# Performance work log

Measured on AMD Instinct MI355X. Metric: run time of the kernel, lower is better.

Reference implementation:

```python
import jax, jax.numpy as jnp
import numpy as np
import math

HEAD_DIM = 64           # d_model // n_heads // 2
N_HEADS = 8
LAMBDA_INIT = 0.8 - 0.6 * math.exp(-0.3 * 6)  # depth=6
EPS = 1e-5


def setup_inputs() -> dict:
    key = jax.random.key(0)
    ks = jax.random.split(key, 8)
    B, T, S = 2, 2048, 2048
    return {
        "queries": jax.random.normal(ks[0], (B, 2 * N_HEADS, T, HEAD_DIM), jnp.float32),
        "keys": jax.random.normal(ks[1], (B, 2 * N_HEADS, S, HEAD_DIM), jnp.float32),
        "values": jax.random.normal(ks[2], (B, N_HEADS, S, 2 * HEAD_DIM), jnp.float32),
        "lambda_q1": 0.02 * jax.random.normal(ks[3], (HEAD_DIM,), jnp.float32),
        "lambda_k1": 0.02 * jax.random.normal(ks[4], (HEAD_DIM,), jnp.float32),
        "lambda_q2": 0.02 * jax.random.normal(ks[5], (HEAD_DIM,), jnp.float32),
        "lambda_k2": 0.02 * jax.random.normal(ks[6], (HEAD_DIM,), jnp.float32),
        "subln_weight": jnp.ones((2 * HEAD_DIM,), jnp.float32),
        "tgt_len": 2048,
        "src_len": 2048,
        "attn_mask": jnp.zeros((1,), jnp.bool_),
    }


def reference(queries, keys, values, lambda_q1, lambda_k1, lambda_q2, lambda_k2,
              subln_weight, tgt_len, src_len, attn_mask):
    B = queries.shape[0]
    scaling = HEAD_DIM ** -0.5
    q = queries * scaling
    # [B, 2H, T, S]
    attn_w = jnp.einsum('bhtd,bhsd->bhts', q, keys)
    attn_w = jax.nn.softmax(attn_w.astype(jnp.float32), axis=-1).astype(queries.dtype)
    lam1 = jnp.exp(jnp.sum(lambda_q1 * lambda_k1))
    lam2 = jnp.exp(jnp.sum(lambda_q2 * lambda_k2))
    lam_full = lam1 - lam2 + LAMBDA_INIT
    attn_w = attn_w.reshape(B, N_HEADS, 2, tgt_len, src_len)
    attn_w = attn_w[:, :, 0] - lam_full * attn_w[:, :, 1]   # [B, H, T, S]
    attn = jnp.einsum('bhts,bhse->bhte', attn_w, values)    # [B, H, T, 2*HEAD_DIM]
    # RMSNorm over last dim
    normed = attn * jax.lax.rsqrt(jnp.mean(jnp.square(attn.astype(jnp.float32)), axis=-1, keepdims=True) + EPS).astype(attn.dtype)
    normed = normed * subln_weight
    out = normed * (1.0 - LAMBDA_INIT)
    out = out.transpose(0, 2, 1, 3).reshape(B, tgt_len, N_HEADS * 2 * HEAD_DIM)
    return out
```

## Files before the change

kernel.cpp:

```cpp
#include <hip/hip_runtime.h>
#include <math.h>


#define NT    2048
#define D     64
#define DV    128
#define TQ    64
#define TS    32
#define NROUND (NT / (2 * TS))

#define LAMBDA_INIT 0.70082066706704814f
#define OUT_SCALE   0.29917933293295186f
#define QSCALE      0.18033688011112042f

typedef __attribute__((ext_vector_type(8)))  short    short8;
typedef __attribute__((ext_vector_type(4)))  short    short4v;
typedef __attribute__((ext_vector_type(8)))  _Float16 half8;
typedef __attribute__((ext_vector_type(2)))  __fp16   fp16x2;
typedef __attribute__((ext_vector_type(4)))  float    f32x4;
typedef unsigned short u16;
typedef unsigned int   u32;

#define MFMAH(a, b, c)  __builtin_amdgcn_mfma_f32_16x16x32_f16(a, b, c, 0, 0, 0)
#define MFMA16(a, b, c) __builtin_amdgcn_mfma_f32_16x16x32_bf16(a, b, c, 0, 0, 0)

#if __has_builtin(__builtin_amdgcn_exp2f)
#define EXP2F(x) __builtin_amdgcn_exp2f(x)
#else
#define EXP2F(x) exp2f(x)
#endif

union Hu { half8 v; _Float16 e[8]; u16 s[8]; short8 sv; };

__device__ __forceinline__ u16 f2h(float x) {
    Hu u; u.e[0] = (_Float16)x; return u.s[0];
}

__device__ __forceinline__ void glds16(const u16* g, const u16* l) {
    __builtin_amdgcn_global_load_lds(
        (const __attribute__((address_space(1))) void*)g,
        (__attribute__((address_space(3))) void*)l, 16, 0, 0);
}

__global__ __launch_bounds__(256) void prep_kv(
    const float* __restrict__ Kg, const float* __restrict__ Vg,
    const float* __restrict__ lq1, const float* __restrict__ lk1,
    const float* __restrict__ lq2, const float* __restrict__ lk2,
    u16* __restrict__ Kf, u16* __restrict__ Vf, float* __restrict__ lamw)
{
    __shared__ u16 th[64 * 136];
    const int bid = blockIdx.x;
    const int t   = threadIdx.x;
    if (bid < 2048) {
        const int idx = (bid * 256 + t) * 8;
        const float4 a = *(const float4*)(Kg + idx);
        const float4 b = *(const float4*)(Kg + idx + 4);
        Hu H;
        H.e[0] = (_Float16)a.x; H.e[1] = (_Float16)a.y;
        H.e[2] = (_Float16)a.z; H.e[3] = (_Float16)a.w;
        H.e[4] = (_Float16)b.x; H.e[5] = (_Float16)b.y;
        H.e[6] = (_Float16)b.z; H.e[7] = (_Float16)b.w;
        *(short8*)(Kf + idx) = H.sv;
        return;
    }
    if (bid == 2048) {
        if (t == 0) {
            float t1 = 0.f, t2 = 0.f;
            for (int i = 0; i < D; ++i) {
                t1 = fmaf(lq1[i], lk1[i], t1);
                t2 = fmaf(lq2[i], lk2[i], t2);
            }
            lamw[0] = __expf(t1) - __expf(t2) + LAMBDA_INIT;
        }
        return;
    }
    const int i  = bid - 2049;
    const int bh = i >> 5;
    const int eb = (i >> 4) & 1;
    const int sb = i & 15;
    const size_t vbase = (size_t)bh * NT * DV + (size_t)sb * 128 * DV + eb * 64;
    {
        const int r0 = t >> 4;
        const int c4 = (t & 15) * 4;
        #pragma unroll
        for (int rr = 0; rr < 8; ++rr) {
            const int row = r0 + rr * 16;
            const float4 x = *(const float4*)(Vg + vbase + (size_t)row * DV + c4);
            th[(c4 + 0) * 136 + row] = f2h(x.x);
            th[(c4 + 1) * 136 + row] = f2h(x.y);
            th[(c4 + 2) * 136 + row] = f2h(x.z);
            th[(c4 + 3) * 136 + row] = f2h(x.w);
        }
    }
    __syncthreads();
    const int e  = t >> 2;
    const int g  = t & 3;
    const size_t orow = ((size_t)bh * DV + eb * 64 + e) * NT + sb * 128;
    #pragma unroll
    for (int c = 0; c < 4; ++c) {
        Hu o;
        #pragma unroll
        for (int j = 0; j < 8; ++j)
            o.s[j] = th[e * 136 + g * 32 + 4 * c + (j & 3) + 16 * (j >> 2)];
        *(short8*)(Vf + orow + g * 32 + c * 8) = o.sv;
    }
}

struct SmemF {
    union {
        short8 c[4096];
        struct {
            float epi[2][32][132];
            float lbuf[2][2][2][32];
        } e;
    };
};

__global__ __launch_bounds__(512, 4) void diffattn_mfma12(
    const float* __restrict__ Qg,
    const u16* __restrict__ Kf, const u16* __restrict__ Vf,
    const float* __restrict__ lamw,
    const float* __restrict__ Wg, float* __restrict__ Outg)
{
    __shared__ SmemF sm;

    const int tid    = threadIdx.x;
    const int wv     = tid >> 6;
    const int lane   = tid & 63;
    const int quad   = lane >> 4;
    const int lc     = lane & 15;
    const int stripe = wv & 1;
    const int hh     = (wv >> 1) & 1;
    const int ks     = wv >> 2;
    const int wig    = wv & 3;
    const int qt     = blockIdx.x;
    const int bh     = blockIdx.y;
    const int b      = bh >> 3, h = bh & 7;

    const int head2b = b * 16 + 2 * h;
    const int bh8    = b * 8 + h;
    const float lam  = lamw[0];

    half8 qf[2][2];
    {
        const size_t qhead = (size_t)(head2b + hh) * NT * D;
        #pragma unroll
        for (int nq = 0; nq < 2; ++nq) {
            const int row = qt * TQ + stripe * 32 + nq * 16 + lc;
            #pragma unroll
            for (int k0 = 0; k0 < 2; ++k0) {
                const int d0 = k0 * 32 + quad * 8;
                const float4 x = *(const float4*)(Qg + qhead + (size_t)row * D + d0);
                const float4 y = *(const float4*)(Qg + qhead + (size_t)row * D + d0 + 4);
                Hu q;
                q.e[0] = (_Float16)(x.x * QSCALE); q.e[1] = (_Float16)(x.y * QSCALE);
                q.e[2] = (_Float16)(x.z * QSCALE); q.e[3] = (_Float16)(x.w * QSCALE);
                q.e[4] = (_Float16)(y.x * QSCALE); q.e[5] = (_Float16)(y.y * QSCALE);
                q.e[6] = (_Float16)(y.z * QSCALE); q.e[7] = (_Float16)(y.w * QSCALE);
                qf[nq][k0] = q.v;
            }
        }
    }

    f32x4 O_[2][8];
    #pragma unroll
    for (int nq = 0; nq < 2; ++nq)
        #pragma unroll
        for (int nt = 0; nt < 8; ++nt) O_[nq][nt] = (f32x4){0.f, 0.f, 0.f, 0.f};
    float lac[2] = {0.f, 0.f};

    u32 kSrc[2], vSrc[2];
    u32 kLds[2], vLds[2];
    #pragma unroll
    for (int t = 0; t < 2; ++t) {
        const int p   = (wig * 2 + t) * 64 + lane;
        const int hhs = p >> 8;
        const int n   = (p >> 3) & 31;
        const int db  = (p & 7) ^ (n & 7);
        kSrc[t] = (u32)(((head2b + hhs) * NT + n) * D + db * 8);
        kLds[t] = (u32)((ks * 512 + (wig * 2 + t) * 64) * 16);
        const int e = p >> 2;
        const int u = (p & 3) ^ ((e >> 1) & 3);
        vSrc[t] = (u32)((bh8 * DV + e) * NT + u * 8);
        vLds[t] = (u32)((1024 + ks * 512 + (wig * 2 + t) * 64) * 16);
    }
    const u16* ldsu = (const u16*)&sm.c[0];

    #pragma unroll
    for (int t = 0; t < 2; ++t) {
        glds16(Kf + kSrc[t] + (u32)ks * (TS * D), ldsu + (kLds[t] >> 1));
        glds16(Vf + vSrc[t] + (u32)ks * TS,       ldsu + (vLds[t] >> 1));
    }
    __syncthreads();

    u32 kOff[2][2];
    #pragma unroll
    for (int k0 = 0; k0 < 2; ++k0)
        #pragma unroll
        for (int mt = 0; mt < 2; ++mt)
            kOff[k0][mt] = (u32)((ks * 512 + hh * 256 + (mt * 16 + lc) * 8 +
                                  ((4 * k0 + quad) ^ (lc & 7))) * 8);
    u32 vOff[8];
    {
        const int swzv = quad ^ ((lc >> 1) & 3);
        #pragma unroll
        for (int nt = 0; nt < 8; ++nt)
            vOff[nt] = (u32)((1024 + ks * 512 + (nt * 16 + lc) * 4 + swzv) * 8);
    }

    const fp16x2 ones = {(__fp16)1.f, (__fp16)1.f};

    for (int r = 0; r < NROUND; ++r) {
        const u32 bo = ((u32)(r & 1)) << 14;

        if (r < NROUND - 1) {
            const u32 tn = (u32)(2 * (r + 1) + ks);
            const u32 ab = ((u32)((r + 1) & 1)) << 14;
            #pragma unroll
            for (int t = 0; t < 2; ++t) {
                glds16(Kf + kSrc[t] + tn * (TS * D), ldsu + ab + (kLds[t] >> 1));
                glds16(Vf + vSrc[t] + tn * TS,       ldsu + ab + (vLds[t] >> 1));
            }
        }

        f32x4 sf[2][2];
        #pragma unroll
        for (int mt = 0; mt < 2; ++mt)
            #pragma unroll
            for (int nq = 0; nq < 2; ++nq) sf[mt][nq] = (f32x4){0.f, 0.f, 0.f, 0.f};
        #pragma unroll
        for (int k0 = 0; k0 < 2; ++k0) {
            #pragma unroll
            for (int mt = 0; mt < 2; ++mt) {
                const half8 kfr = *(const half8*)(ldsu + bo + kOff[k0][mt]);
                #pragma unroll
                for (int nq = 0; nq < 2; ++nq)
                    sf[mt][nq] = MFMAH(kfr, qf[nq][k0], sf[mt][nq]);
            }
        }

        half8 a8[2];
        #pragma unroll
        for (int nq = 0; nq < 2; ++nq) {
            union { half8 v; fp16x2 h[4]; } a;
            float ls = lac[nq];
            #pragma unroll
            for (int mt = 0; mt < 2; ++mt)
                #pragma unroll
                for (int ip = 0; ip < 2; ++ip) {
                    const float p0 = EXP2F(sf[mt][nq][2 * ip]);
                    const float p1 = EXP2F(sf[mt][nq][2 * ip + 1]);
                    const fp16x2 h2 = __builtin_amdgcn_cvt_pkrtz(p0, p1);
                    a.h[mt * 2 + ip] = h2;
                    ls = __builtin_amdgcn_fdot2(h2, ones, ls, false);
                }
            lac[nq] = ls;
            a8[nq] = a.v;
        }

        #pragma unroll
        for (int nt = 0; nt < 8; ++nt) {
            const half8 vfr = *(const half8*)(ldsu + bo + vOff[nt]);
            #pragma unroll
            for (int nq = 0; nq < 2; ++nq)
                O_[nq][nt] = MFMAH(a8[nq], vfr, O_[nq][nt]);
        }

        __syncthreads();
    }

    {
        float s0 = lac[0], s1 = lac[1];
        s0 += __shfl_xor(s0, 16); s0 += __shfl_xor(s0, 32);
        s1 += __shfl_xor(s1, 16); s1 += __shfl_xor(s1, 32);
        if (quad == 0) {
            sm.e.lbuf[hh][ks][stripe][lc]      = s0;
            sm.e.lbuf[hh][ks][stripe][16 + lc] = s1;
        }
    }
    __syncthreads();
    float coef[2][4];
    #pragma unroll
    for (int nq = 0; nq < 2; ++nq)
        #pragma unroll
        for (int i = 0; i < 4; ++i) {
            const int row = nq * 16 + quad * 4 + i;
            const float lt = sm.e.lbuf[hh][0][stripe][row] +
                             sm.e.lbuf[hh][1][stripe][row];
            coef[nq][i] = (hh == 0) ? (1.f / lt) : (-lam / lt);
        }
    __syncthreads();
    const int pid = hh * 2 + ks;
    #pragma unroll
    for (int p = 0; p < 4; ++p) {
        if (pid == p) {
            #pragma unroll
            for (int nq = 0; nq < 2; ++nq)
                #pragma unroll
                for (int i = 0; i < 4; ++i) {
                    const int row = nq * 16 + quad * 4 + i;
                    #pragma unroll
                    for (int nt = 0; nt < 8; ++nt) {
                        const int col = nt * 16 + lc;
                        const float v = O_[nq][nt][i] * coef[nq][i];
                        if (p == 0) sm.e.epi[stripe][row][col] = v;
                        else        sm.e.epi[stripe][row][col] += v;
                    }
                }
        }
        __syncthreads();
    }
    {
        const int r0 = wv * 8 + (lane >> 3);
        const int st = r0 >> 5, ri = r0 & 31;
        const int e0 = (lane & 7) * 16;
        float x[16];
        float ssq = 0.f;
        #pragma unroll
        for (int m = 0; m < 16; m += 4) {
            const float4 t4 = *(const float4*)&sm.e.epi[st][ri][e0 + m];
            x[m] = t4.x; x[m + 1] = t4.y; x[m + 2] = t4.z; x[m + 3] = t4.w;
            ssq += t4.x * t4.x + t4.y * t4.y + t4.z * t4.z + t4.w * t4.w;
        }
        ssq += __shfl_xor(ssq, 1);
        ssq += __shfl_xor(ssq, 2);
        ssq += __shfl_xor(ssq, 4);
        const float rsq = rsqrtf(ssq * (1.f / 128.f) + 1e-5f) * OUT_SCALE;
        const int rowg = qt * TQ + r0;
        const size_t base =
            ((size_t)b * NT + rowg) * (size_t)(8 * DV) + (size_t)h * DV;
        #pragma unroll
        for (int m = 0; m < 16; m += 4) {
            const float4 w4 = *(const float4*)(Wg + e0 + m);
            float4 o4;
            o4.x = x[m] * rsq * w4.x;
            o4.y = x[m + 1] * rsq * w4.y;
            o4.z = x[m + 2] * rsq * w4.z;
            o4.w = x[m + 3] * rsq * w4.w;
            *(float4*)(Outg + base + e0 + m) = o4;
        }
    }
}

__device__ __forceinline__ unsigned short f2bf(float x) {
    unsigned u = __float_as_uint(x);
    return (unsigned short)((u + 0x7fffu + ((u >> 16) & 1u)) >> 16);
}
__device__ __forceinline__ float bf2f(unsigned short h) {
    return __uint_as_float(((unsigned)h) << 16);
}

struct SmemB {
    union {
        struct {
            short8 kh[2][264];
            short8 kl[2][264];
            short8 vh[516];
            short8 vl[516];
            unsigned short ph[2][2560];
            unsigned short pl[2][2560];
        } L;
        float epi[2][32][132];
    };
};

__global__ __launch_bounds__(256, 2) void diffattn_fb(
    const float* __restrict__ Qg, const float* __restrict__ Kg,
    const float* __restrict__ Vg,
    const float* __restrict__ lq1, const float* __restrict__ lk1,
    const float* __restrict__ lq2, const float* __restrict__ lk2,
    const float* __restrict__ Wg, float* __restrict__ Outg)
{
    __shared__ SmemB sm;
    const int tid = threadIdx.x;
    const int wv = tid >> 6, lane = tid & 63;
    const int quad = lane >> 4, lc = lane & 15;
    const int stripe = wv & 1, hh = wv >> 1;
    const int qt = blockIdx.x, bh = blockIdx.y;
    const int b = bh >> 3, h = bh & 7;
    const size_t koff0 = ((size_t)(b * 16 + 2 * h)) * NT * D;
    const size_t voff  = ((size_t)(b * 8 + h)) * NT * DV;
    float t1 = 0.f, t2 = 0.f;
    for (int i = 0; i < D; ++i) {
        t1 = fmaf(lq1[i], lk1[i], t1);
        t2 = fmaf(lq2[i], lk2[i], t2);
    }
    const float lam = __expf(t1) - __expf(t2) + LAMBDA_INIT;
    short8 qfh[2][2], qfl[2][2];
    {
        const size_t qhead = ((size_t)(b * 16 + 2 * h + hh)) * NT * D;
        #pragma unroll
        for (int mt = 0; mt < 2; ++mt)
            #pragma unroll
            for (int k0 = 0; k0 < 2; ++k0) {
                const int row = qt * TQ + stripe * 32 + mt * 16 + lc;
                const int d0  = k0 * 32 + quad * 8;
                const float4 x = *(const float4*)(Qg + qhead + (size_t)row * D + d0);
                const float4 y = *(const float4*)(Qg + qhead + (size_t)row * D + d0 + 4);
                float f[8] = {x.x, x.y, x.z, x.w, y.x, y.y, y.z, y.w};
                #pragma unroll
                for (int j = 0; j < 8; ++j) {
                    const float v = f[j] * 0.125f;
                    const unsigned short hi = f2bf(v);
                    qfh[mt][k0][j] = (short)hi;
                    qfl[mt][k0][j] = (short)f2bf(v - bf2f(hi));
                }
            }
    }
    f32x4 O_[2][8];
    #pragma unroll
    for (int mt = 0; mt < 2; ++mt)
        #pragma unroll
        for (int nt = 0; nt < 8; ++nt) O_[mt][nt] = (f32x4){0.f, 0.f, 0.f, 0.f};
    float m_[2][4], l_[2][4], a_[2][4];
    #pragma unroll
    for (int mt = 0; mt < 2; ++mt)
        #pragma unroll
        for (int i = 0; i < 4; ++i) { m_[mt][i] = -1e30f; l_[mt][i] = 0.f; }
    const int s_hh = tid >> 7;
    const int s_n  = (tid >> 2) & 31;
    const int s_d0 = (tid & 3) * 16;
    const int s_e0 = tid & 31;
    const int s_s0 = ((tid >> 5) & 7) * 4;
    const int s_sb = s_s0 >> 3;
    const int s_hs = (s_s0 & 4) ? 1 : 0;
    for (int kt = 0; kt < NT / TS; ++kt) {
        const int kb = kt * TS;
        __syncthreads();
        {
            const float* kp = Kg + koff0 + (size_t)s_hh * NT * D +
                              (size_t)(kb + s_n) * D + s_d0;
            const float4 x0 = ((const float4*)kp)[0];
            const float4 x1 = ((const float4*)kp)[1];
            const float4 x2 = ((const float4*)kp)[2];
            const float4 x3 = ((const float4*)kp)[3];
            float f[16] = {x0.x, x0.y, x0.z, x0.w, x1.x, x1.y, x1.z, x1.w,
                           x2.x, x2.y, x2.z, x2.w, x3.x, x3.y, x3.z, x3.w};
            short8 c0h, c0l, c1h, c1l;
            #pragma unroll
            for (int j = 0; j < 8; ++j) {
                unsigned short hi = f2bf(f[j]);
                c0h[j] = (short)hi; c0l[j] = (short)f2bf(f[j] - bf2f(hi));
                hi = f2bf(f[8 + j]);
                c1h[j] = (short)hi; c1l[j] = (short)f2bf(f[8 + j] - bf2f(hi));
            }
            const int db0 = s_d0 >> 3;
            sm.L.kh[s_hh][db0 * 33 + s_n]       = c0h;
            sm.L.kl[s_hh][db0 * 33 + s_n]       = c0l;
            sm.L.kh[s_hh][(db0 + 1) * 33 + s_n] = c1h;
            sm.L.kl[s_hh][(db0 + 1) * 33 + s_n] = c1l;
        }
        {
            #pragma unroll
            for (int j = 0; j < 4; ++j) {
                const int e = s_e0 + 32 * j;
                float f[4];
                #pragma unroll
                for (int i = 0; i < 4; ++i)
                    f[i] = Vg[voff + (size_t)(kb + s_s0 + i) * DV + e];
                short4v hi4, lo4;
                #pragma unroll
                for (int i = 0; i < 4; ++i) {
                    const unsigned short hi = f2bf(f[i]);
                    hi4[i] = (short)hi;
                    lo4[i] = (short)f2bf(f[i] - bf2f(hi));
                }
                ((short4v*)&sm.L.vh[s_sb * 129 + e])[s_hs] = hi4;
                ((short4v*)&sm.L.vl[s_sb * 129 + e])[s_hs] = lo4;
            }
        }
        __syncthreads();
        f32x4 s_f[2][2];
        #pragma unroll
        for (int mt = 0; mt < 2; ++mt)
            #pragma unroll
            for (int nt = 0; nt < 2; ++nt) s_f[mt][nt] = (f32x4){0.f, 0.f, 0.f, 0.f};
        #pragma unroll
        for (int k0 = 0; k0 < 2; ++k0)
            #pragma unroll
            for (int nt = 0; nt < 2; ++nt) {
                const short8 kh = sm.L.kh[hh][(4 * k0 + quad) * 33 + nt * 16 + lc];
                const short8 kl = sm.L.kl[hh][(4 * k0 + quad) * 33 + nt * 16 + lc];
                #pragma unroll
                for (int mt = 0; mt < 2; ++mt) {
                    s_f[mt][nt] = MFMA16(qfh[mt][k0], kh, s_f[mt][nt]);
                    s_f[mt][nt] = MFMA16(qfl[mt][k0], kh, s_f[mt][nt]);
                    s_f[mt][nt] = MFMA16(qfh[mt][k0], kl, s_f[mt][nt]);
                }
            }
        #pragma unroll
        for (int mt = 0; mt < 2; ++mt)
            #pragma unroll
            for (int i = 0; i < 4; ++i) {
                const float v0 = s_f[mt][0][i], v1 = s_f[mt][1][i];
                float mx = fmaxf(v0, v1);
                mx = fmaxf(mx, __shfl_xor(mx, 1));
                mx = fmaxf(mx, __shfl_xor(mx, 2));
                mx = fmaxf(mx, __shfl_xor(mx, 4));
                mx = fmaxf(mx, __shfl_xor(mx, 8));
                const float mn = fmaxf(m_[mt][i], mx);
                const float al = __expf(m_[mt][i] - mn);
                const float p0 = __expf(v0 - mn);
                const float p1 = __expf(v1 - mn);
                float rs = p0 + p1;
                rs += __shfl_xor(rs, 1);
                rs += __shfl_xor(rs, 2);
                rs += __shfl_xor(rs, 4);
                rs += __shfl_xor(rs, 8);
                l_[mt][i] = l_[mt][i] * al + rs;
                m_[mt][i] = mn;
                a_[mt][i] = al;
                const int r = stripe * 32 + mt * 16 + quad * 4 + i;
                const unsigned short h0 = f2bf(p0);
                sm.L.ph[hh][r * 40 + lc]      = h0;
                sm.L.pl[hh][r * 40 + lc]      = f2bf(p0 - bf2f(h0));
                const unsigned short h1 = f2bf(p1);
                sm.L.ph[hh][r * 40 + 16 + lc] = h1;
                sm.L.pl[hh][r * 40 + 16 + lc] = f2bf(p1 - bf2f(h1));
            }
        __syncthreads();
        #pragma unroll
        for (int mt = 0; mt < 2; ++mt)
            #pragma unroll
            for (int nt = 0; nt < 8; ++nt)
                #pragma unroll
                for (int i = 0; i < 4; ++i) O_[mt][nt][i] *= a_[mt][i];
        short8 pah[2], pal[2];
        #pragma unroll
        for (int mt = 0; mt < 2; ++mt) {
            const int r = stripe * 32 + mt * 16 + lc;
            pah[mt] = *(const short8*)&sm.L.ph[hh][r * 40 + quad * 8];
            pal[mt] = *(const short8*)&sm.L.pl[hh][r * 40 + quad * 8];
        }
        #pragma unroll
        for (int nt = 0; nt < 8; ++nt) {
            const short8 vh = sm.L.vh[quad * 129 + nt * 16 + lc];
            const short8 vl = sm.L.vl[quad * 129 + nt * 16 + lc];
            #pragma unroll
            for (int mt = 0; mt < 2; ++mt) {
                O_[mt][nt] = MFMA16(pah[mt], vh, O_[mt][nt]);
                O_[mt][nt] = MFMA16(pal[mt], vh, O_[mt][nt]);
                O_[mt][nt] = MFMA16(pah[mt], vl, O_[mt][nt]);
            }
        }
    }
    __syncthreads();
    if (hh == 1) {
        #pragma unroll
        for (int mt = 0; mt < 2; ++mt)
            #pragma unroll
            for (int i = 0; i < 4; ++i) {
                const float inv = lam / l_[mt][i];
                const int r = mt * 16 + quad * 4 + i;
                #pragma unroll
                for (int nt = 0; nt < 8; ++nt)
                    sm.epi[stripe][r][nt * 16 + lc] = O_[mt][nt][i] * inv;
            }
    }
    __syncthreads();
    if (hh == 0) {
        float wvv[8];
        #pragma unroll
        for (int nt = 0; nt < 8; ++nt) wvv[nt] = Wg[nt * 16 + lc];
        #pragma unroll
        for (int mt = 0; mt < 2; ++mt)
            #pragma unroll
            for (int i = 0; i < 4; ++i) {
                const float inv1 = 1.f / l_[mt][i];
                const int r = mt * 16 + quad * 4 + i;
                float od[8];
                float ss = 0.f;
                #pragma unroll
                for (int nt = 0; nt < 8; ++nt) {
                    od[nt] = O_[mt][nt][i] * inv1 - sm.epi[stripe][r][nt * 16 + lc];
                    ss = fmaf(od[nt], od[nt], ss);
                }
                ss += __shfl_xor(ss, 1);
                ss += __shfl_xor(ss, 2);
                ss += __shfl_xor(ss, 4);
                ss += __shfl_xor(ss, 8);
                const float rsq = rsqrtf(ss * (1.f / 128.f) + 1e-5f) * OUT_SCALE;
                const int rowg = qt * TQ + stripe * 32 + r;
                const size_t base =
                    ((size_t)b * NT + rowg) * (size_t)(8 * DV) + (size_t)h * DV;
                #pragma unroll
                for (int nt = 0; nt < 8; ++nt)
                    Outg[base + nt * 16 + lc] = od[nt] * rsq * wvv[nt];
            }
    }
}

extern "C" void kernel_launch(void* const* d_in, const int* in_sizes, int n_in,
                              void* d_out, int out_size, void* d_ws, size_t ws_size,
                              hipStream_t stream) {
    const float* Q   = (const float*)d_in[0];
    const float* K   = (const float*)d_in[1];
    const float* V   = (const float*)d_in[2];
    const float* lq1 = (const float*)d_in[3];
    const float* lk1 = (const float*)d_in[4];
    const float* lq2 = (const float*)d_in[5];
    const float* lk2 = (const float*)d_in[6];
    const float* W   = (const float*)d_in[7];
    float* Out = (float*)d_out;
    const size_t NEED = 2ull * 4194304ull * sizeof(u16) + 16;
    if (ws_size >= NEED) {
        u16*   Kf   = (u16*)d_ws;
        u16*   Vf   = Kf + 4194304;
        float* lamw = (float*)(Vf + 4194304);
        prep_kv<<<2561, 256, 0, stream>>>(K, V, lq1, lk1, lq2, lk2, Kf, Vf, lamw);
        diffattn_mfma12<<<dim3(NT / TQ, 16), 512, 0, stream>>>(
            Q, Kf, Vf, lamw, W, Out);
    } else {
        diffattn_fb<<<dim3(NT / TQ, 16), 256, 0, stream>>>(
            Q, K, V, lq1, lk1, lq2, lk2, W, Out);
    }
}
```

Before: 169.6 us.

## Pre-swizzle K/V into MFMA fragment order and load directly from global

```diff
diff --git a/kernel.cpp b/kernel.cpp
--- a/kernel.cpp
+++ b/kernel.cpp
@@ -34,12 +34,6 @@
 
 __device__ __forceinline__ u16 f2h(float x) {
     Hu u; u.e[0] = (_Float16)x; return u.s[0];
-}
-
-__device__ __forceinline__ void glds16(const u16* g, const u16* l) {
-    __builtin_amdgcn_global_load_lds(
-        (const __attribute__((address_space(1))) void*)g,
-        (__attribute__((address_space(3))) void*)l, 16, 0, 0);
 }
 
 __global__ __launch_bounds__(256) void prep_kv(
@@ -51,19 +45,50 @@
     __shared__ u16 th[64 * 136];
     const int bid = blockIdx.x;
     const int t   = threadIdx.x;
-    if (bid < 2048) {
-        const int idx = (bid * 256 + t) * 8;
-        const float4 a = *(const float4*)(Kg + idx);
-        const float4 b = *(const float4*)(Kg + idx + 4);
-        Hu H;
-        H.e[0] = (_Float16)a.x; H.e[1] = (_Float16)a.y;
-        H.e[2] = (_Float16)a.z; H.e[3] = (_Float16)a.w;
-        H.e[4] = (_Float16)b.x; H.e[5] = (_Float16)b.y;
-        H.e[6] = (_Float16)b.z; H.e[7] = (_Float16)b.w;
-        *(short8*)(Kf + idx) = H.sv;
+    if (bid < 1024) {
+        const int bh2 = bid >> 5;
+        const int tp  = bid & 31;
+        {
+            const int key = t >> 2;
+            const int d0  = (t & 3) * 16;
+            const float* src =
+                Kg + ((size_t)bh2 * NT + (size_t)tp * 64 + key) * D + d0;
+            const float4 x0 = ((const float4*)src)[0];
+            const float4 x1 = ((const float4*)src)[1];
+            const float4 x2 = ((const float4*)src)[2];
+            const float4 x3 = ((const float4*)src)[3];
+            Hu a, b;
+            a.e[0] = (_Float16)x0.x; a.e[1] = (_Float16)x0.y;
+            a.e[2] = (_Float16)x0.z; a.e[3] = (_Float16)x0.w;
+            a.e[4] = (_Float16)x1.x; a.e[5] = (_Float16)x1.y;
+            a.e[6] = (_Float16)x1.z; a.e[7] = (_Float16)x1.w;
+            b.e[0] = (_Float16)x2.x; b.e[1] = (_Float16)x2.y;
+            b.e[2] = (_Float16)x2.z; b.e[3] = (_Float16)x2.w;
+            b.e[4] = (_Float16)x3.x; b.e[5] = (_Float16)x3.y;
+            b.e[6] = (_Float16)x3.z; b.e[7] = (_Float16)x3.w;
+            *(short8*)(th + key * 80 + d0)     = a.sv;
+            *(short8*)(th + key * 80 + d0 + 8) = b.sv;
+        }
+        __syncthreads();
+        #pragma unroll
+        for (int q = 0; q < 2; ++q) {
+            const int c    = t * 2 + q;
+            const int tt   = c >> 8;
+            const int k0   = (c >> 7) & 1;
+            const int mt   = (c >> 6) & 1;
+            const int lane = c & 63;
+            const int qd   = lane >> 4, lcl = lane & 15;
+            const short8 o =
+                *(const short8*)(th + (tt * 32 + mt * 16 + lcl) * 80 +
+                                 k0 * 32 + qd * 8);
+            const size_t oc =
+                (((size_t)(bh2 * 64 + tp * 2 + tt)) * 4 + k0 * 2 + mt) * 512 +
+                lane * 8;
+            *(short8*)(Kf + oc) = o;
+        }
         return;
     }
-    if (bid == 2048) {
+    if (bid == 1024) {
         if (t == 0) {
             float t1 = 0.f, t2 = 0.f;
             for (int i = 0; i < D; ++i) {
@@ -74,7 +99,7 @@
         }
         return;
     }
-    const int i  = bid - 2049;
+    const int i  = bid - 1025;
     const int bh = i >> 5;
     const int eb = (i >> 4) & 1;
     const int sb = i & 15;
@@ -93,36 +118,37 @@
         }
     }
     __syncthreads();
-    const int e  = t >> 2;
-    const int g  = t & 3;
-    const size_t orow = ((size_t)bh * DV + eb * 64 + e) * NT + sb * 128;
     #pragma unroll
-    for (int c = 0; c < 4; ++c) {
-        Hu o;
+    for (int q = 0; q < 4; ++q) {
+        const int o    = t * 4 + q;
+        const int gt   = o >> 8;
+        const int ntl  = (o >> 6) & 3;
+        const int lane = o & 63;
+        const int cq   = lane >> 4, lcl = lane & 15;
+        const int el   = ntl * 16 + lcl;
+        Hu ov;
         #pragma unroll
         for (int j = 0; j < 8; ++j)
-            o.s[j] = th[e * 136 + g * 32 + 4 * c + (j & 3) + 16 * (j >> 2)];
-        *(short8*)(Vf + orow + g * 32 + c * 8) = o.sv;
+            ov.s[j] = th[el * 136 + gt * 32 + 4 * cq + (j & 3) + 16 * (j >> 2)];
+        const size_t oc =
+            (((size_t)(bh * 64 + sb * 4 + gt)) * 8 + eb * 4 + ntl) * 512 +
+            lane * 8;
+        *(short8*)(Vf + oc) = ov.sv;
     }
 }
 
-struct SmemF {
-    union {
-        short8 c[4096];
-        struct {
-            float epi[2][32][132];
-            float lbuf[2][2][2][32];
-        } e;
-    };
+struct SmemE {
+    float epi[2][32][132];
+    float lbuf[2][2][2][32];
 };
 
-__global__ __launch_bounds__(512, 4) void diffattn_mfma12(
+__global__ __launch_bounds__(512, 4) void diffattn_mfma13(
     const float* __restrict__ Qg,
     const u16* __restrict__ Kf, const u16* __restrict__ Vf,
     const float* __restrict__ lamw,
     const float* __restrict__ Wg, float* __restrict__ Outg)
 {
-    __shared__ SmemF sm;
+    __shared__ SmemE sm;
 
     const int tid    = threadIdx.x;
     const int wv     = tid >> 6;
@@ -132,18 +158,18 @@
     const int stripe = wv & 1;
     const int hh     = (wv >> 1) & 1;
     const int ks     = wv >> 2;
-    const int wig    = wv & 3;
     const int qt     = blockIdx.x;
     const int bh     = blockIdx.y;
     const int b      = bh >> 3, h = bh & 7;
 
     const int head2b = b * 16 + 2 * h;
     const int bh8    = b * 8 + h;
+    const int bh2    = head2b + hh;
     const float lam  = lamw[0];
 
     half8 qf[2][2];
     {
-        const size_t qhead = (size_t)(head2b + hh) * NT * D;
+        const size_t qhead = (size_t)bh2 * NT * D;
         #pragma unroll
         for (int nq = 0; nq < 2; ++nq) {
             const int row = qt * TQ + stripe * 32 + nq * 16 + lc;
@@ -169,75 +195,35 @@
         for (int nt = 0; nt < 8; ++nt) O_[nq][nt] = (f32x4){0.f, 0.f, 0.f, 0.f};
     float lac[2] = {0.f, 0.f};
 
-    u32 kSrc[2], vSrc[2];
-    u32 kLds[2], vLds[2];
-    #pragma unroll
-    for (int t = 0; t < 2; ++t) {
-        const int p   = (wig * 2 + t) * 64 + lane;
-        const int hhs = p >> 8;
-        const int n   = (p >> 3) & 31;
-        const int db  = (p & 7) ^ (n & 7);
-        kSrc[t] = (u32)(((head2b + hhs) * NT + n) * D + db * 8);
-        kLds[t] = (u32)((ks * 512 + (wig * 2 + t) * 64) * 16);
-        const int e = p >> 2;
-        const int u = (p & 3) ^ ((e >> 1) & 3);
-        vSrc[t] = (u32)((bh8 * DV + e) * NT + u * 8);
-        vLds[t] = (u32)((1024 + ks * 512 + (wig * 2 + t) * 64) * 16);
-    }
-    const u16* ldsu = (const u16*)&sm.c[0];
-
-    #pragma unroll
-    for (int t = 0; t < 2; ++t) {
-        glds16(Kf + kSrc[t] + (u32)ks * (TS * D), ldsu + (kLds[t] >> 1));
-        glds16(Vf + vSrc[t] + (u32)ks * TS,       ldsu + (vLds[t] >> 1));
-    }
-    __syncthreads();
-
-    u32 kOff[2][2];
-    #pragma unroll
-    for (int k0 = 0; k0 < 2; ++k0)
-        #pragma unroll
-        for (int mt = 0; mt < 2; ++mt)
-            kOff[k0][mt] = (u32)((ks * 512 + hh * 256 + (mt * 16 + lc) * 8 +
-                                  ((4 * k0 + quad) ^ (lc & 7))) * 8);
-    u32 vOff[8];
-    {
-        const int swzv = quad ^ ((lc >> 1) & 3);
-        #pragma unroll
-        for (int nt = 0; nt < 8; ++nt)
-            vOff[nt] = (u32)((1024 + ks * 512 + (nt * 16 + lc) * 4 + swzv) * 8);
-    }
+    const u32 kbase = (u32)(bh2 * 64) * 2048 + (u32)(lane * 8);
+    const u32 vbase = (u32)(bh8 * 64) * 4096 + (u32)(lane * 8);
 
     const fp16x2 ones = {(__fp16)1.f, (__fp16)1.f};
+    const f32x4  z4   = {0.f, 0.f, 0.f, 0.f};
 
     for (int r = 0; r < NROUND; ++r) {
-        const u32 bo = ((u32)(r & 1)) << 14;
-
-        if (r < NROUND - 1) {
-            const u32 tn = (u32)(2 * (r + 1) + ks);
-            const u32 ab = ((u32)((r + 1) & 1)) << 14;
-            #pragma unroll
-            for (int t = 0; t < 2; ++t) {
-                glds16(Kf + kSrc[t] + tn * (TS * D), ldsu + ab + (kLds[t] >> 1));
-                glds16(Vf + vSrc[t] + tn * TS,       ldsu + ab + (vLds[t] >> 1));
-            }
-        }
+        const u32 t_ = (u32)(2 * r + ks);
+        const u16* kp = Kf + kbase + t_ * 2048;
+        const u16* vp = Vf + vbase + t_ * 4096;
+
+        half8 kfr[2][2];
+        #pragma unroll
+        for (int k0 = 0; k0 < 2; ++k0)
+            #pragma unroll
+            for (int mt = 0; mt < 2; ++mt)
+                kfr[k0][mt] = *(const half8*)(kp + (k0 * 2 + mt) * 512);
 
         f32x4 sf[2][2];
         #pragma unroll
         for (int mt = 0; mt < 2; ++mt)
             #pragma unroll
-            for (int nq = 0; nq < 2; ++nq) sf[mt][nq] = (f32x4){0.f, 0.f, 0.f, 0.f};
-        #pragma unroll
-        for (int k0 = 0; k0 < 2; ++k0) {
-            #pragma unroll
-            for (int mt = 0; mt < 2; ++mt) {
-                const half8 kfr = *(const half8*)(ldsu + bo + kOff[k0][mt]);
-                #pragma unroll
-                for (int nq = 0; nq < 2; ++nq)
-                    sf[mt][nq] = MFMAH(kfr, qf[nq][k0], sf[mt][nq]);
-            }
-        }
+            for (int nq = 0; nq < 2; ++nq)
+                sf[mt][nq] = MFMAH(kfr[0][mt], qf[nq][0], z4);
+        #pragma unroll
+        for (int mt = 0; mt < 2; ++mt)
+            #pragma unroll
+            for (int nq = 0; nq < 2; ++nq)
+                sf[mt][nq] = MFMAH(kfr[1][mt], qf[nq][1], sf[mt][nq]);
 
         half8 a8[2];
         #pragma unroll
@@ -259,14 +245,17 @@
         }
 
         #pragma unroll
-        for (int nt = 0; nt < 8; ++nt) {
-            const half8 vfr = *(const half8*)(ldsu + bo + vOff[nt]);
-            #pragma unroll
-            for (int nq = 0; nq < 2; ++nq)
-                O_[nq][nt] = MFMAH(a8[nq], vfr, O_[nq][nt]);
-        }
-
-        __syncthreads();
+        for (int g = 0; g < 2; ++g) {
+            half8 vfr[4];
+            #pragma unroll
+            for (int n = 0; n < 4; ++n)
+                vfr[n] = *(const half8*)(vp + (g * 4 + n) * 512);
+            #pragma unroll
+            for (int n = 0; n < 4; ++n)
+                #pragma unroll
+                for (int nq = 0; nq < 2; ++nq)
+                    O_[nq][g * 4 + n] = MFMAH(a8[nq], vfr[n], O_[nq][g * 4 + n]);
+        }
     }
 
     {
@@ -274,8 +263,8 @@
         s0 += __shfl_xor(s0, 16); s0 += __shfl_xor(s0, 32);
         s1 += __shfl_xor(s1, 16); s1 += __shfl_xor(s1, 32);
         if (quad == 0) {
-            sm.e.lbuf[hh][ks][stripe][lc]      = s0;
-            sm.e.lbuf[hh][ks][stripe][16 + lc] = s1;
+            sm.lbuf[hh][ks][stripe][lc]      = s0;
+            sm.lbuf[hh][ks][stripe][16 + lc] = s1;
         }
     }
     __syncthreads();
@@ -285,8 +274,8 @@
         #pragma unroll
         for (int i = 0; i < 4; ++i) {
             const int row = nq * 16 + quad * 4 + i;
-            const float lt = sm.e.lbuf[hh][0][stripe][row] +
-                             sm.e.lbuf[hh][1][stripe][row];
+            const float lt = sm.lbuf[hh][0][stripe][row] +
+                             sm.lbuf[hh][1][stripe][row];
             coef[nq][i] = (hh == 0) ? (1.f / lt) : (-lam / lt);
         }
     __syncthreads();
@@ -303,8 +292,8 @@
                     for (int nt = 0; nt < 8; ++nt) {
                         const int col = nt * 16 + lc;
                         const float v = O_[nq][nt][i] * coef[nq][i];
-                        if (p == 0) sm.e.epi[stripe][row][col] = v;
-                        else        sm.e.epi[stripe][row][col] += v;
+                        if (p == 0) sm.epi[stripe][row][col] = v;
+                        else        sm.epi[stripe][row][col] += v;
                     }
                 }
         }
@@ -318,7 +307,7 @@
         float ssq = 0.f;
         #pragma unroll
         for (int m = 0; m < 16; m += 4) {
-            const float4 t4 = *(const float4*)&sm.e.epi[st][ri][e0 + m];
+            const float4 t4 = *(const float4*)&sm.epi[st][ri][e0 + m];
             x[m] = t4.x; x[m + 1] = t4.y; x[m + 2] = t4.z; x[m + 3] = t4.w;
             ssq += t4.x * t4.x + t4.y * t4.y + t4.z * t4.z + t4.w * t4.w;
         }
@@ -607,8 +596,8 @@
         u16*   Kf   = (u16*)d_ws;
         u16*   Vf   = Kf + 4194304;
         float* lamw = (float*)(Vf + 4194304);
-        prep_kv<<<2561, 256, 0, stream>>>(K, V, lq1, lk1, lq2, lk2, Kf, Vf, lamw);
-        diffattn_mfma12<<<dim3(NT / TQ, 16), 512, 0, stream>>>(
+        prep_kv<<<1537, 256, 0, stream>>>(K, V, lq1, lk1, lq2, lk2, Kf, Vf, lamw);
+        diffattn_mfma13<<<dim3(NT / TQ, 16), 512, 0, stream>>>(
             Q, Kf, Vf, lamw, W, Out);
     } else {
         diffattn_fb<<<dim3(NT / TQ, 16), 256, 0, stream>>>(
```

Result: no change. 168.9 us (-0.4%).

## Pre-swizzle V into MFMA fragment order and load it directly from global

Applied to the files above, without the earlier changes.

```diff
diff --git a/kernel.cpp b/kernel.cpp
--- a/kernel.cpp
+++ b/kernel.cpp
@@ -93,22 +93,28 @@
         }
     }
     __syncthreads();
-    const int e  = t >> 2;
-    const int g  = t & 3;
-    const size_t orow = ((size_t)bh * DV + eb * 64 + e) * NT + sb * 128;
-    #pragma unroll
-    for (int c = 0; c < 4; ++c) {
-        Hu o;
+    #pragma unroll
+    for (int q = 0; q < 4; ++q) {
+        const int o    = t * 4 + q;
+        const int gt   = o >> 8;
+        const int ntl  = (o >> 6) & 3;
+        const int lane = o & 63;
+        const int cq   = lane >> 4, lcl = lane & 15;
+        const int el   = ntl * 16 + lcl;
+        Hu ov;
         #pragma unroll
         for (int j = 0; j < 8; ++j)
-            o.s[j] = th[e * 136 + g * 32 + 4 * c + (j & 3) + 16 * (j >> 2)];
-        *(short8*)(Vf + orow + g * 32 + c * 8) = o.sv;
+            ov.s[j] = th[el * 136 + gt * 32 + 4 * cq + (j & 3) + 16 * (j >> 2)];
+        const size_t oc =
+            (((size_t)(bh * 64 + sb * 4 + gt)) * 8 + eb * 4 + ntl) * 512 +
+            lane * 8;
+        *(short8*)(Vf + oc) = ov.sv;
     }
 }
 
 struct SmemF {
     union {
-        short8 c[4096];
+        short8 c[2048];
         struct {
             float epi[2][32][132];
             float lbuf[2][2][2][32];
@@ -116,7 +122,7 @@
     };
 };
 
-__global__ __launch_bounds__(512, 4) void diffattn_mfma12(
+__global__ __launch_bounds__(512, 4) void diffattn_mfma14(
     const float* __restrict__ Qg,
     const u16* __restrict__ Kf, const u16* __restrict__ Vf,
     const float* __restrict__ lamw,
@@ -139,11 +145,12 @@
 
     const int head2b = b * 16 + 2 * h;
     const int bh8    = b * 8 + h;
+    const int bh2    = head2b + hh;
     const float lam  = lamw[0];
 
     half8 qf[2][2];
     {
-        const size_t qhead = (size_t)(head2b + hh) * NT * D;
+        const size_t qhead = (size_t)bh2 * NT * D;
         #pragma unroll
         for (int nq = 0; nq < 2; ++nq) {
             const int row = qt * TQ + stripe * 32 + nq * 16 + lc;
@@ -169,8 +176,8 @@
         for (int nt = 0; nt < 8; ++nt) O_[nq][nt] = (f32x4){0.f, 0.f, 0.f, 0.f};
     float lac[2] = {0.f, 0.f};
 
-    u32 kSrc[2], vSrc[2];
-    u32 kLds[2], vLds[2];
+    u32 kSrc[2];
+    u32 kLds[2];
     #pragma unroll
     for (int t = 0; t < 2; ++t) {
         const int p   = (wig * 2 + t) * 64 + lane;
@@ -179,18 +186,12 @@
         const int db  = (p & 7) ^ (n & 7);
         kSrc[t] = (u32)(((head2b + hhs) * NT + n) * D + db * 8);
         kLds[t] = (u32)((ks * 512 + (wig * 2 + t) * 64) * 16);
-        const int e = p >> 2;
-        const int u = (p & 3) ^ ((e >> 1) & 3);
-        vSrc[t] = (u32)((bh8 * DV + e) * NT + u * 8);
-        vLds[t] = (u32)((1024 + ks * 512 + (wig * 2 + t) * 64) * 16);
     }
     const u16* ldsu = (const u16*)&sm.c[0];
 
     #pragma unroll
-    for (int t = 0; t < 2; ++t) {
+    for (int t = 0; t < 2; ++t)
         glds16(Kf + kSrc[t] + (u32)ks * (TS * D), ldsu + (kLds[t] >> 1));
-        glds16(Vf + vSrc[t] + (u32)ks * TS,       ldsu + (vLds[t] >> 1));
-    }
     __syncthreads();
 
     u32 kOff[2][2];
@@ -200,27 +201,22 @@
         for (int mt = 0; mt < 2; ++mt)
             kOff[k0][mt] = (u32)((ks * 512 + hh * 256 + (mt * 16 + lc) * 8 +
                                   ((4 * k0 + quad) ^ (lc & 7))) * 8);
-    u32 vOff[8];
-    {
-        const int swzv = quad ^ ((lc >> 1) & 3);
-        #pragma unroll
-        for (int nt = 0; nt < 8; ++nt)
-            vOff[nt] = (u32)((1024 + ks * 512 + (nt * 16 + lc) * 4 + swzv) * 8);
-    }
+
+    const u32 vbase = (u32)(bh8 * 64) * 4096 + (u32)(lane * 8);
 
     const fp16x2 ones = {(__fp16)1.f, (__fp16)1.f};
 
     for (int r = 0; r < NROUND; ++r) {
-        const u32 bo = ((u32)(r & 1)) << 14;
+        const u32 bo = ((u32)(r & 1)) << 13;
+        const u32 t_ = (u32)(2 * r + ks);
+        const u16* vp = Vf + vbase + t_ * 4096;
 
         if (r < NROUND - 1) {
             const u32 tn = (u32)(2 * (r + 1) + ks);
-            const u32 ab = ((u32)((r + 1) & 1)) << 14;
-            #pragma unroll
-            for (int t = 0; t < 2; ++t) {
+            const u32 ab = ((u32)((r + 1) & 1)) << 13;
+            #pragma unroll
+            for (int t = 0; t < 2; ++t)
                 glds16(Kf + kSrc[t] + tn * (TS * D), ldsu + ab + (kLds[t] >> 1));
-                glds16(Vf + vSrc[t] + tn * TS,       ldsu + ab + (vLds[t] >> 1));
-            }
         }
 
         f32x4 sf[2][2];
@@ -259,11 +255,18 @@
         }
 
         #pragma unroll
-        for (int nt = 0; nt < 8; ++nt) {
-            const half8 vfr = *(const half8*)(ldsu + bo + vOff[nt]);
-            #pragma unroll
-            for (int nq = 0; nq < 2; ++nq)
-                O_[nq][nt] = MFMAH(a8[nq], vfr, O_[nq][nt]);
+        for (int g = 0; g < 2; ++g) {
+            half8 vfr[4];
+            #pragma unroll
+            for (int n = 0; n < 4; ++n)
+                vfr[n] = *(const half8*)(vp + (g * 4 + n) * 512);
+            __builtin_amdgcn_s_setprio(1);
+            #pragma unroll
+            for (int n = 0; n < 4; ++n)
+                #pragma unroll
+                for (int nq = 0; nq < 2; ++nq)
+                    O_[nq][g * 4 + n] = MFMAH(a8[nq], vfr[n], O_[nq][g * 4 + n]);
+            __builtin_amdgcn_s_setprio(0);
         }
 
         __syncthreads();
@@ -608,7 +611,7 @@
         u16*   Vf   = Kf + 4194304;
         float* lamw = (float*)(Vf + 4194304);
         prep_kv<<<2561, 256, 0, stream>>>(K, V, lq1, lk1, lq2, lk2, Kf, Vf, lamw);
-        diffattn_mfma12<<<dim3(NT / TQ, 16), 512, 0, stream>>>(
+        diffattn_mfma14<<<dim3(NT / TQ, 16), 512, 0, stream>>>(
             Q, Kf, Vf, lamw, W, Out);
     } else {
         diffattn_fb<<<dim3(NT / TQ, 16), 256, 0, stream>>>(
```

New measurement: 171.8 us. About the same (+1.3%).
